# Optimization experiments

Hardware: AMD Instinct MI355X
Metric: run time of the kernel (lower is better)

Reference implementation:

```python
import jax, jax.numpy as jnp
import numpy as np

N = 50000      # nodes
E = 800000     # edges (avg degree 16)
IN, H, OUT = 128, 128, 64


def setup_inputs() -> dict:
    key = jax.random.key(0)
    k1, k2, k3, k4 = jax.random.split(key, 4)
    x = jax.random.normal(k1, (N, IN), dtype=jnp.float32)
    edge_index = jax.random.randint(k2, (2, E), 0, N, dtype=jnp.int32)
    W1 = jax.random.normal(k3, (IN, H), dtype=jnp.float32) * (1.0 / np.sqrt(IN))
    b1 = jnp.zeros((H,), dtype=jnp.float32)
    W2 = jax.random.normal(k4, (H, OUT), dtype=jnp.float32) * (1.0 / np.sqrt(H))
    b2 = jnp.zeros((OUT,), dtype=jnp.float32)
    return {"x": x, "edge_index": edge_index, "W1": W1, "b1": b1, "W2": W2, "b2": b2}


def gcn_conv(x, edge_index, W, b):
    """PyG GCNConv: D^-1/2 (A + I) D^-1/2 (x W) + b, with self-loops."""
    src, dst = edge_index[0], edge_index[1]
    h = x @ W                                              # [N, F_out] transform first (F_out <= F_in path)
    ones = jnp.ones((src.shape[0],), dtype=h.dtype)
    deg = jax.ops.segment_sum(ones, dst, num_segments=N) + 1.0  # +1 for self-loop
    inv_sqrt_deg = jax.lax.rsqrt(deg)
    norm = inv_sqrt_deg[src] * inv_sqrt_deg[dst]           # [E]
    agg = jax.ops.segment_sum(h[src] * norm[:, None], dst, num_segments=N)
    # self-loop contribution: norm_ii = deg_i^-1
    return agg + h * (1.0 / deg)[:, None] + b


def reference(x, edge_index, W1, b1, W2, b2):
    h = jax.nn.relu(gcn_conv(x, edge_index, W1, b1))
    return gcn_conv(h, edge_index, W2, b2)
```

## Files before the change

### kernel.cpp

```cpp
#include <hip/hip_runtime.h>
#include <hip/hip_bf16.h>


#define GCN_IN   128
#define GCN_H    128
#define GCN_OUT  64
#define CAP      64
#define OVF_CAP  32768
#define SPILL_CAP 65536
#define PASSA_BLOCKS 256
#define SEG_CAP  24
#define MAXBUCK  512

using short8 = __attribute__((ext_vector_type(8))) short;
using f32x4  = __attribute__((ext_vector_type(4))) float;
using int4v  = __attribute__((ext_vector_type(4))) int;

__device__ __forceinline__ ushort f2bf(float f) {
    uint b = __float_as_uint(f);
    b = (b + 0x7FFFu + ((b >> 16) & 1u)) >> 16;
    return (ushort)b;
}
__device__ __forceinline__ float bf2f_lo(uint u) { return __uint_as_float(u << 16); }
__device__ __forceinline__ float bf2f_hi(uint u) { return __uint_as_float(u & 0xFFFF0000u); }

__global__ __launch_bounds__(256) void k_fused1(
        const int* __restrict__ src, const int* __restrict__ dst,
        uint* __restrict__ seg, ushort* __restrict__ cntAB,
        int* __restrict__ spillcnt, uint* __restrict__ spill, int E,
        const float* __restrict__ A, const float* __restrict__ B,
        ushort* __restrict__ C, int M, int N) {
    __shared__ __align__(16) ushort As[64][40];
    __shared__ __align__(16) ushort Bs[128][40];
    __shared__ int cntL[MAXBUCK];
    const int tid = threadIdx.x;
    const int nb  = (N + 127) >> 7;

    if (blockIdx.x < PASSA_BLOCKS) {
        const int blk = blockIdx.x;
        for (int i = tid; i < nb; i += 256) cntL[i] = 0;
        __syncthreads();
        const int stride4 = PASSA_BLOCKS * 256 * 4;
        for (int e = (blk * 256 + tid) * 4; e < E; e += stride4) {
            int4v d4 = __builtin_nontemporal_load((const int4v*)(dst + e));
            int4v s4 = __builtin_nontemporal_load((const int4v*)(src + e));
            #pragma unroll
            for (int k = 0; k < 4; ++k) {
                int d = d4[k];
                int s = s4[k];
                int b = d >> 7;
                int pos = atomicAdd(&cntL[b], 1);
                if (pos < SEG_CAP) {
                    seg[((size_t)b * PASSA_BLOCKS + blk) * SEG_CAP + pos] =
                        ((uint)d << 16) | (uint)s;
                } else {
                    int q = atomicAdd(spillcnt, 1);
                    if (q < SPILL_CAP) spill[q] = ((uint)d << 16) | (uint)s;
                }
            }
        }
        __syncthreads();
        for (int b = tid; b < nb; b += 256)
            cntAB[(size_t)b * PASSA_BLOCKS + blk] = (ushort)min(cntL[b], SEG_CAP);
        return;
    }

    const int g    = blockIdx.x - PASSA_BLOCKS;
    const int row0 = g * 64;
    const int w    = tid >> 6;
    const int lane = tid & 63;
    const int l15  = lane & 15;
    const int q8   = (lane >> 4) * 8;

    f32x4 acc[8];
    #pragma unroll
    for (int t = 0; t < 8; ++t) {
        acc[t][0] = 0.f; acc[t][1] = 0.f; acc[t][2] = 0.f; acc[t][3] = 0.f;
    }
    for (int kb = 0; kb < 128; kb += 32) {
        #pragma unroll
        for (int tt = 0; tt < 2; ++tt) {
            int f = tid * 4 + tt * 1024;
            int r = f >> 5;
            int k = f & 31;
            float4 v = make_float4(0.f, 0.f, 0.f, 0.f);
            int gr = row0 + r;
            if (gr < M) v = *(const float4*)(A + (size_t)gr * 128 + kb + k);
            ushort4 o;
            o.x = f2bf(v.x); o.y = f2bf(v.y); o.z = f2bf(v.z); o.w = f2bf(v.w);
            *(ushort4*)&As[r][k] = o;
        }
        #pragma unroll
        for (int tt = 0; tt < 4; ++tt) {
            int f = tid * 4 + tt * 1024;
            int k = f >> 7;
            int n = f & 127;
            float4 v = *(const float4*)(B + (size_t)(kb + k) * 128 + n);
            Bs[n + 0][k] = f2bf(v.x);
            Bs[n + 1][k] = f2bf(v.y);
            Bs[n + 2][k] = f2bf(v.z);
            Bs[n + 3][k] = f2bf(v.w);
        }
        __syncthreads();
        short8 a = *(const short8*)&As[16 * w + l15][q8];
        #pragma unroll
        for (int t = 0; t < 8; ++t) {
            short8 b = *(const short8*)&Bs[16 * t + l15][q8];
            acc[t] = __builtin_amdgcn_mfma_f32_16x16x32_bf16(a, b, acc[t], 0, 0, 0);
        }
        __syncthreads();
    }
    const int quad = lane >> 4;
    #pragma unroll
    for (int r = 0; r < 4; ++r) {
        int grow = row0 + 16 * w + quad * 4 + r;
        if (grow < M) {
            #pragma unroll
            for (int t = 0; t < 8; ++t) {
                __builtin_nontemporal_store(
                    f2bf(acc[t][r]), C + (size_t)grow * 128 + 16 * t + l15);
            }
        }
    }
}

__global__ __launch_bounds__(256) void k_passB(const uint* __restrict__ seg,
                                               const ushort* __restrict__ cntAB,
                                               const int* __restrict__ spillcnt,
                                               const uint* __restrict__ spill,
                                               int* __restrict__ cnt,
                                               ushort* __restrict__ slot,
                                               int* __restrict__ ovfcnt,
                                               int2* __restrict__ ovf, int N) {
    __shared__ int cntL[128];
    const int tid  = threadIdx.x;
    const int b    = blockIdx.x;
    const int base = b << 7;
    if (tid < 128) cntL[tid] = 0;
    __syncthreads();

    const int cs = (int)cntAB[(size_t)b * PASSA_BLOCKS + tid];
    const uint* sp = seg + ((size_t)b * PASSA_BLOCKS + tid) * SEG_CAP;
    for (int c4 = 0; c4 < SEG_CAP; c4 += 4) {
        if (c4 >= cs) break;
        uint4 v = *(const uint4*)(sp + c4);
        const uint* vv = (const uint*)&v;
        #pragma unroll
        for (int k = 0; k < 4; ++k) {
            int idx = c4 + k;
            if (idx < cs) {
                uint pr = vv[k];
                int d = (int)(pr >> 16);
                int s = (int)(pr & 0xFFFFu);
                int pos = atomicAdd(&cntL[d - base], 1);
                if (pos < CAP) {
                    slot[(size_t)d * CAP + pos] = (ushort)s;
                } else {
                    int q = atomicAdd(ovfcnt, 1);
                    if (q < OVF_CAP) ovf[q] = make_int2(d, s);
                }
            }
        }
    }
    const int spn = min(*spillcnt, SPILL_CAP);
    for (int t = tid; t < spn; t += 256) {
        uint pr = spill[t];
        int d = (int)(pr >> 16);
        if (d >= base && d < base + 128) {
            int s = (int)(pr & 0xFFFFu);
            int pos = atomicAdd(&cntL[d - base], 1);
            if (pos < CAP) {
                slot[(size_t)d * CAP + pos] = (ushort)s;
            } else {
                int q = atomicAdd(ovfcnt, 1);
                if (q < OVF_CAP) ovf[q] = make_int2(d, s);
            }
        }
    }
    __syncthreads();
    if (tid < 128) {
        int d = base + tid;
        if (d < N) {
            int c = cntL[tid];
            if (c) cnt[d] += c;
        }
    }
}

__global__ __launch_bounds__(256) void k_agg128(const ushort* __restrict__ h,
                                                const int* __restrict__ cnt,
                                                const ushort* __restrict__ slot,
                                                const float* __restrict__ bias,
                                                const int* __restrict__ ovfcnt,
                                                const int2* __restrict__ ovf,
                                                ushort* __restrict__ out, int n) {
    int node = (blockIdx.x * 256 + threadIdx.x) >> 6;
    int lane = threadIdx.x & 63;
    if (node >= n) return;
    int deg = cnt[node];
    int degm = min(deg, CAP);
    float isd_i = rsqrtf((float)(deg + 1));
    int sidx = (int)__builtin_nontemporal_load(slot + (size_t)node * CAP + lane);
    bool valid = lane < degm;
    if (!valid) sidx = 0;
    float wl = valid ? rsqrtf((float)(cnt[sidx] + 1)) : 0.f;

    const int q = lane >> 4;
    const int i = lane & 15;
    const ushort* hp = h + 8 * i;

    float acc[8] = {};
    for (int j = 0; j < degm; j += 8) {
        int j0 = j + q;
        int j1 = j + 4 + q;
        int   s0 = __shfl(sidx, j0);
        int   s1 = __shfl(sidx, j1);
        float w0 = __shfl(wl, j0);
        float w1 = __shfl(wl, j1);
        uint4 v0 = *(const uint4*)(hp + (size_t)s0 * 128);
        uint4 v1 = *(const uint4*)(hp + (size_t)s1 * 128);
        acc[0] += w0 * bf2f_lo(v0.x) + w1 * bf2f_lo(v1.x);
        acc[1] += w0 * bf2f_hi(v0.x) + w1 * bf2f_hi(v1.x);
        acc[2] += w0 * bf2f_lo(v0.y) + w1 * bf2f_lo(v1.y);
        acc[3] += w0 * bf2f_hi(v0.y) + w1 * bf2f_hi(v1.y);
        acc[4] += w0 * bf2f_lo(v0.z) + w1 * bf2f_lo(v1.z);
        acc[5] += w0 * bf2f_hi(v0.z) + w1 * bf2f_hi(v1.z);
        acc[6] += w0 * bf2f_lo(v0.w) + w1 * bf2f_lo(v1.w);
        acc[7] += w0 * bf2f_hi(v0.w) + w1 * bf2f_hi(v1.w);
    }
    int ovn = *ovfcnt;
    for (int t = 0; t < ovn; ++t) {
        int2 p = ovf[t];
        if (p.x == node && q == 0) {
            float w0 = rsqrtf((float)(cnt[p.y] + 1));
            uint4 v0 = *(const uint4*)(hp + (size_t)p.y * 128);
            acc[0] += w0 * bf2f_lo(v0.x); acc[1] += w0 * bf2f_hi(v0.x);
            acc[2] += w0 * bf2f_lo(v0.y); acc[3] += w0 * bf2f_hi(v0.y);
            acc[4] += w0 * bf2f_lo(v0.z); acc[5] += w0 * bf2f_hi(v0.z);
            acc[6] += w0 * bf2f_lo(v0.w); acc[7] += w0 * bf2f_hi(v0.w);
        }
    }
    #pragma unroll
    for (int k = 0; k < 8; ++k) {
        acc[k] += __shfl_xor(acc[k], 16);
        acc[k] += __shfl_xor(acc[k], 32);
    }
    if (q == 0) {
        uint4 vs = *(const uint4*)(hp + (size_t)node * 128);
        float4 ba = *(const float4*)(bias + 8 * i);
        float4 bb = *(const float4*)(bias + 8 * i + 4);
        float r0 = fmaxf((acc[0] + isd_i * bf2f_lo(vs.x)) * isd_i + ba.x, 0.f);
        float r1 = fmaxf((acc[1] + isd_i * bf2f_hi(vs.x)) * isd_i + ba.y, 0.f);
        float r2 = fmaxf((acc[2] + isd_i * bf2f_lo(vs.y)) * isd_i + ba.z, 0.f);
        float r3 = fmaxf((acc[3] + isd_i * bf2f_hi(vs.y)) * isd_i + ba.w, 0.f);
        float r4 = fmaxf((acc[4] + isd_i * bf2f_lo(vs.z)) * isd_i + bb.x, 0.f);
        float r5 = fmaxf((acc[5] + isd_i * bf2f_hi(vs.z)) * isd_i + bb.y, 0.f);
        float r6 = fmaxf((acc[6] + isd_i * bf2f_lo(vs.w)) * isd_i + bb.z, 0.f);
        float r7 = fmaxf((acc[7] + isd_i * bf2f_hi(vs.w)) * isd_i + bb.w, 0.f);
        uint4 o;
        o.x = (uint)f2bf(r0) | ((uint)f2bf(r1) << 16);
        o.y = (uint)f2bf(r2) | ((uint)f2bf(r3) << 16);
        o.z = (uint)f2bf(r4) | ((uint)f2bf(r5) << 16);
        o.w = (uint)f2bf(r6) | ((uint)f2bf(r7) << 16);
        *(uint4*)(out + (size_t)node * 128 + 8 * i) = o;
    }
}

__global__ __launch_bounds__(256) void k_gemm2(const ushort* __restrict__ A,
                                               const float* __restrict__ B,
                                               const int* __restrict__ cnt,
                                               ushort* __restrict__ C, int M) {
    __shared__ __align__(16) ushort As[64][136];
    __shared__ __align__(16) ushort Bs[64][136];
    const int tid  = threadIdx.x;
    const int w    = tid >> 6;
    const int lane = tid & 63;
    const int l15  = lane & 15;
    const int q8   = (lane >> 4) * 8;
    const int row0 = blockIdx.x * 64;

    #pragma unroll
    for (int t = 0; t < 4; ++t) {
        int f = tid * 8 + t * 2048;
        int r = f >> 7;
        int k = f & 127;
        uint4 v = make_uint4(0u, 0u, 0u, 0u);
        int gr = row0 + r;
        if (gr < M) v = *(const uint4*)(A + (size_t)gr * 128 + k);
        *(uint4*)&As[r][k] = v;
    }
    #pragma unroll
    for (int t = 0; t < 8; ++t) {
        int f = tid * 4 + t * 1024;
        int k = f >> 6;
        int n = f & 63;
        float4 v = *(const float4*)(B + (size_t)k * 64 + n);
        Bs[n + 0][k] = f2bf(v.x);
        Bs[n + 1][k] = f2bf(v.y);
        Bs[n + 2][k] = f2bf(v.z);
        Bs[n + 3][k] = f2bf(v.w);
    }
    __syncthreads();

    f32x4 acc[4];
    #pragma unroll
    for (int t = 0; t < 4; ++t) {
        acc[t][0] = 0.f; acc[t][1] = 0.f; acc[t][2] = 0.f; acc[t][3] = 0.f;
    }
    #pragma unroll
    for (int kt = 0; kt < 4; ++kt) {
        short8 a = *(const short8*)&As[16 * w + l15][32 * kt + q8];
        #pragma unroll
        for (int t = 0; t < 4; ++t) {
            short8 b = *(const short8*)&Bs[16 * t + l15][32 * kt + q8];
            acc[t] = __builtin_amdgcn_mfma_f32_16x16x32_bf16(a, b, acc[t], 0, 0, 0);
        }
    }
    const int quad = lane >> 4;
    #pragma unroll
    for (int r = 0; r < 4; ++r) {
        int grow = row0 + 16 * w + quad * 4 + r;
        if (grow < M) {
            float ws = rsqrtf((float)(cnt[grow] + 1));
            #pragma unroll
            for (int t = 0; t < 4; ++t) {
                C[(size_t)grow * 64 + 16 * t + l15] = f2bf(ws * acc[t][r]);
            }
        }
    }
}

__global__ __launch_bounds__(256) void k_agg64(const ushort* __restrict__ h,
                                               const int* __restrict__ cnt,
                                               const ushort* __restrict__ slot,
                                               const float* __restrict__ bias,
                                               const int* __restrict__ ovfcnt,
                                               const int2* __restrict__ ovf,
                                               float* __restrict__ out, int n) {
    int node = (blockIdx.x * 256 + threadIdx.x) >> 6;
    int lane = threadIdx.x & 63;
    if (node >= n) return;
    int deg = cnt[node];
    int degm = min(deg, CAP);
    float isd_i = rsqrtf((float)(deg + 1));
    int sidx = (int)__builtin_nontemporal_load(slot + (size_t)node * CAP + lane);

    const int g = lane >> 3;
    const int i = lane & 7;
    const ushort* hp = h + 8 * i;

    float acc[8] = {};
    for (int j = 0; j < degm; j += 16) {
        int j0 = j + g;
        int j1 = j + 8 + g;
        int   s0 = __shfl(sidx, j0);
        int   s1 = __shfl(sidx, j1);
        float w0 = (j0 < degm) ? 1.f : 0.f;
        float w1 = (j1 < degm) ? 1.f : 0.f;
        uint4 v0 = *(const uint4*)(hp + (size_t)s0 * 64);
        uint4 v1 = *(const uint4*)(hp + (size_t)s1 * 64);
        acc[0] += w0 * bf2f_lo(v0.x) + w1 * bf2f_lo(v1.x);
        acc[1] += w0 * bf2f_hi(v0.x) + w1 * bf2f_hi(v1.x);
        acc[2] += w0 * bf2f_lo(v0.y) + w1 * bf2f_lo(v1.y);
        acc[3] += w0 * bf2f_hi(v0.y) + w1 * bf2f_hi(v1.y);
        acc[4] += w0 * bf2f_lo(v0.z) + w1 * bf2f_lo(v1.z);
        acc[5] += w0 * bf2f_hi(v0.z) + w1 * bf2f_hi(v1.z);
        acc[6] += w0 * bf2f_lo(v0.w) + w1 * bf2f_lo(v1.w);
        acc[7] += w0 * bf2f_hi(v0.w) + w1 * bf2f_hi(v1.w);
    }
    int ovn = *ovfcnt;
    for (int t = 0; t < ovn; ++t) {
        int2 p = ovf[t];
        if (p.x == node && g == 0) {
            uint4 v0 = *(const uint4*)(hp + (size_t)p.y * 64);
            acc[0] += bf2f_lo(v0.x); acc[1] += bf2f_hi(v0.x);
            acc[2] += bf2f_lo(v0.y); acc[3] += bf2f_hi(v0.y);
            acc[4] += bf2f_lo(v0.z); acc[5] += bf2f_hi(v0.z);
            acc[6] += bf2f_lo(v0.w); acc[7] += bf2f_hi(v0.w);
        }
    }
    #pragma unroll
    for (int k = 0; k < 8; ++k) {
        acc[k] += __shfl_xor(acc[k], 8);
        acc[k] += __shfl_xor(acc[k], 16);
        acc[k] += __shfl_xor(acc[k], 32);
    }
    if (g == 0) {
        uint4 vs = *(const uint4*)(hp + (size_t)node * 64);
        float4 ba = *(const float4*)(bias + 8 * i);
        float4 bb = *(const float4*)(bias + 8 * i + 4);
        float4 r0, r1;
        r0.x = (acc[0] + bf2f_lo(vs.x)) * isd_i + ba.x;
        r0.y = (acc[1] + bf2f_hi(vs.x)) * isd_i + ba.y;
        r0.z = (acc[2] + bf2f_lo(vs.y)) * isd_i + ba.z;
        r0.w = (acc[3] + bf2f_hi(vs.y)) * isd_i + ba.w;
        r1.x = (acc[4] + bf2f_lo(vs.z)) * isd_i + bb.x;
        r1.y = (acc[5] + bf2f_hi(vs.z)) * isd_i + bb.y;
        r1.z = (acc[6] + bf2f_lo(vs.w)) * isd_i + bb.z;
        r1.w = (acc[7] + bf2f_hi(vs.w)) * isd_i + bb.w;
        float* op = out + (size_t)node * 64 + 8 * i;
        *(float4*)op = r0;
        *(float4*)(op + 4) = r1;
    }
}

static inline size_t align256(size_t x) { return (x + 255) & ~(size_t)255; }
static inline size_t maxsz(size_t a, size_t b) { return a > b ? a : b; }

extern "C" void kernel_launch(void* const* d_in, const int* in_sizes, int n_in,
                              void* d_out, int out_size, void* d_ws, size_t ws_size,
                              hipStream_t stream) {
    const float* x  = (const float*)d_in[0];
    const int*   ei = (const int*)d_in[1];
    const float* W1 = (const float*)d_in[2];
    const float* b1 = (const float*)d_in[3];
    const float* W2 = (const float*)d_in[4];
    const float* b2 = (const float*)d_in[5];
    float* out = (float*)d_out;

    const int N = in_sizes[0] / GCN_IN;
    const int E = in_sizes[1] / 2;
    const int* src = ei;
    const int* dst = ei + E;
    const int nb = (N + 127) >> 7;

    char* ws = (char*)d_ws;
    size_t o = 0;
    int*    cnt     = (int*)(ws + o);    o += align256((size_t)N * 4);
    int*    ovfcnt  = (int*)(ws + o);
    int*    spillcnt = ovfcnt + 1;       o += 256;
    int2*   ovf     = (int2*)(ws + o);   o += align256((size_t)OVF_CAP * 8);
    uint*   spill   = (uint*)(ws + o);   o += align256((size_t)SPILL_CAP * 4);
    ushort* slot    = (ushort*)(ws + o); o += align256((size_t)N * CAP * 2);
    ushort* hb      = (ushort*)(ws + o); o += align256((size_t)N * GCN_H * 2);
    size_t seg_sz   = align256((size_t)nb * PASSA_BLOCKS * SEG_CAP * 4);
    size_t cntab_sz = align256((size_t)nb * PASSA_BLOCKS * 2);
    size_t h1_sz    = align256((size_t)N * GCN_H * 2);
    char*  zone     = ws + o;            o += maxsz(seg_sz + cntab_sz, h1_sz);
    uint*   seg    = (uint*)zone;
    ushort* cntAB  = (ushort*)(zone + seg_sz);
    ushort* h1b    = (ushort*)zone;
    ushort* h2b    = (ushort*)(ws + o);  o += align256((size_t)N * GCN_OUT * 2);

    (void)hipMemsetAsync(cnt, 0, align256((size_t)N * 4) + 256, stream);

    {
        int gemm_blocks = (N + 63) / 64;
        k_fused1<<<PASSA_BLOCKS + gemm_blocks, 256, 0, stream>>>(
            src, dst, seg, cntAB, spillcnt, spill, E, x, W1, hb, N, N);
    }

    k_passB<<<nb, 256, 0, stream>>>(seg, cntAB, spillcnt, spill, cnt, slot,
                                    ovfcnt, ovf, N);

    k_agg128<<<(N * 64 + 255) / 256, 256, 0, stream>>>(hb, cnt, slot, b1,
                                                       ovfcnt, ovf, h1b, N);

    k_gemm2<<<(N + 63) / 64, 256, 0, stream>>>(h1b, W2, cnt, h2b, N);

    k_agg64<<<(N * 64 + 255) / 256, 256, 0, stream>>>(h2b, cnt, slot, b2,
                                                      ovfcnt, ovf, out, N);
}
```

Baseline: 176.4 us.

## Counting-sort edges in shared memory before writing bucket segments

The edge-bucketing blocks now make two passes over their edge slice. The first builds a per-bucket histogram and a prefix scan; the second scatters packed (dst,src) pairs into a shared-memory sorted buffer, which is then written to the global segment array in bucket order. This replaces scattered global stores with more contiguous, coalesced writes. The cost is a second read of dst, extra shared-memory traffic and barriers, and a fixed 4096-entry sort buffer that assumes each block's slice fits. The GEMM tiles now alias the same shared buffer.

```diff
diff --git a/kernel.cpp b/kernel.cpp
--- a/kernel.cpp
+++ b/kernel.cpp
@@ -10,7 +10,7 @@
 #define SPILL_CAP 65536
 #define PASSA_BLOCKS 256
 #define SEG_CAP  24
-#define MAXBUCK  512
+#define SORT_CAP 4096
 
 using short8 = __attribute__((ext_vector_type(8))) short;
 using f32x4  = __attribute__((ext_vector_type(4))) float;
@@ -30,41 +30,82 @@
         int* __restrict__ spillcnt, uint* __restrict__ spill, int E,
         const float* __restrict__ A, const float* __restrict__ B,
         ushort* __restrict__ C, int M, int N) {
-    __shared__ __align__(16) ushort As[64][40];
-    __shared__ __align__(16) ushort Bs[128][40];
-    __shared__ int cntL[MAXBUCK];
+    __shared__ __align__(16) uint smemU[5760];
     const int tid = threadIdx.x;
     const int nb  = (N + 127) >> 7;
 
     if (blockIdx.x < PASSA_BLOCKS) {
+        uint* histL  = smemU;
+        uint* scanEx = smemU + 512;
+        uint* hist2  = smemU + 1024;
+        uint* sorted = smemU + 1536;
+        uint* totalS = smemU + 1536 + SORT_CAP;
+
         const int blk = blockIdx.x;
-        for (int i = tid; i < nb; i += 256) cntL[i] = 0;
+        const int stride4 = PASSA_BLOCKS * 256 * 4;
+        for (int i = tid; i < 512; i += 256) { histL[i] = 0; hist2[i] = 0; }
         __syncthreads();
-        const int stride4 = PASSA_BLOCKS * 256 * 4;
+
+        for (int e = (blk * 256 + tid) * 4; e < E; e += stride4) {
+            int4v d4 = __builtin_nontemporal_load((const int4v*)(dst + e));
+            #pragma unroll
+            for (int k = 0; k < 4; ++k) atomicAdd(&histL[d4[k] >> 7], 1u);
+        }
+        __syncthreads();
+
+        if (tid < 64) {
+            int base = tid * 8;
+            uint loc[8];
+            uint run = 0;
+            #pragma unroll
+            for (int j = 0; j < 8; ++j) { loc[j] = run; run += histL[base + j]; }
+            uint inc = run;
+            #pragma unroll
+            for (int d = 1; d < 64; d <<= 1) {
+                uint v = __shfl_up(inc, d, 64);
+                if (tid >= d) inc += v;
+            }
+            uint exc = inc - run;
+            #pragma unroll
+            for (int j = 0; j < 8; ++j) scanEx[base + j] = exc + loc[j];
+            if (tid == 63) totalS[0] = inc;
+        }
+        __syncthreads();
+
+        for (int b = tid; b < nb; b += 256)
+            cntAB[(size_t)b * PASSA_BLOCKS + blk] =
+                (ushort)min((int)histL[b], SEG_CAP);
+
         for (int e = (blk * 256 + tid) * 4; e < E; e += stride4) {
             int4v d4 = __builtin_nontemporal_load((const int4v*)(dst + e));
             int4v s4 = __builtin_nontemporal_load((const int4v*)(src + e));
             #pragma unroll
             for (int k = 0; k < 4; ++k) {
                 int d = d4[k];
-                int s = s4[k];
                 int b = d >> 7;
-                int pos = atomicAdd(&cntL[b], 1);
-                if (pos < SEG_CAP) {
-                    seg[((size_t)b * PASSA_BLOCKS + blk) * SEG_CAP + pos] =
-                        ((uint)d << 16) | (uint)s;
-                } else {
-                    int q = atomicAdd(spillcnt, 1);
-                    if (q < SPILL_CAP) spill[q] = ((uint)d << 16) | (uint)s;
-                }
+                uint r = atomicAdd(&hist2[b], 1u);
+                sorted[scanEx[b] + r] = ((uint)d << 16) | (uint)s4[k];
             }
         }
         __syncthreads();
-        for (int b = tid; b < nb; b += 256)
-            cntAB[(size_t)b * PASSA_BLOCKS + blk] = (ushort)min(cntL[b], SEG_CAP);
+
+        const int myE = (int)totalS[0];
+        for (int i = tid; i < myE; i += 256) {
+            uint pr = sorted[i];
+            int b = (int)(pr >> 23);
+            int gpos = i - (int)scanEx[b];
+            if (gpos < SEG_CAP) {
+                seg[((size_t)b * PASSA_BLOCKS + blk) * SEG_CAP + gpos] = pr;
+            } else {
+                int q = atomicAdd(spillcnt, 1);
+                if (q < SPILL_CAP) spill[q] = pr;
+            }
+        }
         return;
     }
 
+    ushort (*As)[40] = (ushort (*)[40])(smemU);
+    ushort (*Bs)[40] = (ushort (*)[40])(smemU + 1280);
     const int g    = blockIdx.x - PASSA_BLOCKS;
     const int row0 = g * 64;
     const int w    = tid >> 6;
```

After: 176.3 us. No clear change (-0.1%).
